# Optimization experiments

Hardware: AMD Instinct MI355X
Metric: run time of the kernel (lower is better)

## Reference

```python
import jax, jax.numpy as jnp
import numpy as np

N_NODES = 50000
N_EDGES = 400000
NFEAT, NHID, NOUT, NCLASS = 512, 256, 256, 8


def _glorot(key, shape):
    lim = float(np.sqrt(6.0 / (shape[0] + shape[1])))
    return jax.random.uniform(key, shape, jnp.float32, -lim, lim)


def setup_inputs() -> dict:
    key = jax.random.key(0)
    ks = jax.random.split(key, 8)
    x = jax.random.normal(ks[0], (N_NODES, NFEAT), jnp.float32)
    edge_index = jax.random.randint(ks[1], (2, N_EDGES), 0, N_NODES, jnp.int32)
    # learnable edge weight logits (init 1 - eps in the module; trained => generic values)
    edge_w_params = jnp.ones((N_EDGES,), jnp.float32) * 0.9999
    W1 = _glorot(ks[2], (NFEAT, NHID)); b1 = jnp.zeros((NHID,), jnp.float32)
    W2 = _glorot(ks[3], (NHID, NHID)); b2 = jnp.zeros((NHID,), jnp.float32)
    W3 = _glorot(ks[4], (NHID, NOUT)); b3 = jnp.zeros((NOUT,), jnp.float32)
    Wlin = _glorot(ks[5], (NHID + NHID + NOUT, NCLASS))
    blin = jnp.zeros((NCLASS,), jnp.float32)
    return {"x": x, "edge_index": edge_index, "edge_w_params": edge_w_params,
            "W1": W1, "b1": b1, "W2": W2, "b2": b2, "W3": W3, "b3": b3,
            "Wlin": Wlin, "blin": blin}


def _gcn_conv(x, W, b, src, dst, ew, n):
    """PyG GCNConv with add_self_loops=True.
    Self-loop weight is 1 (fill_value). norm = d^-1/2[src] * w * d^-1/2[dst].
    Self-loop contribution handled analytically (no edge concat).
    """
    deg = jax.ops.segment_sum(ew, dst, num_segments=n) + 1.0  # +1 self-loop weight
    dinv = jnp.where(deg > 0, jax.lax.rsqrt(deg), 0.0)
    norm = dinv[src] * ew * dinv[dst]                          # [E]
    h = x @ W                                                  # [n, out]
    agg = jax.ops.segment_sum(h[src] * norm[:, None], dst, num_segments=n)
    agg = agg + h * (dinv * dinv)[:, None]                     # self loops
    return agg + b


def reference(x, edge_index, edge_w_params, W1, b1, W2, b2, W3, b3, Wlin, blin):
    n = x.shape[0]
    src, dst = edge_index[0], edge_index[1]
    ew = jax.nn.sigmoid(edge_w_params)
    ones_ew = jnp.ones_like(ew)
    x1 = jax.nn.relu(_gcn_conv(x, W1, b1, src, dst, ew, n))    # dropout: eval mode (identity)
    x2 = jax.nn.relu(_gcn_conv(x1, W2, b2, src, dst, ew, n))
    x3 = _gcn_conv(x2, W3, b3, src, dst, ones_ew, n)           # gc3 called without edge_weight
    logits = jnp.concatenate((x1, x2, x3), axis=1) @ Wlin + blin
    return jax.nn.log_softmax(logits, axis=1)
```

## Files before the change

kernel.cpp:

```cpp
#include <hip/hip_runtime.h>
#include <math.h>

#define N_NODES 50000
#define N_EDGES 400000
#define M_PAD 50048
#define NFEAT 512
#define NHID 256
#define NCLASS 8
#define SCAN_BLOCKS ((N_NODES + 255) / 256)

typedef unsigned short u16;
typedef __attribute__((ext_vector_type(8))) unsigned short u16x8;
typedef __attribute__((ext_vector_type(8))) short s16x8;
typedef __attribute__((ext_vector_type(4))) float f32x4;

__device__ __forceinline__ float bf2f(u16 u) {
    union { unsigned int i; float f; } v; v.i = ((unsigned int)u) << 16; return v.f;
}
__device__ __forceinline__ float bf2f_hi(unsigned int packed) {
    union { unsigned int i; float f; } v; v.i = packed & 0xffff0000u; return v.f;
}
__device__ __forceinline__ float bf2f_lo(unsigned int packed) {
    union { unsigned int i; float f; } v; v.i = packed << 16; return v.f;
}
__device__ __forceinline__ u16 f2bf(float f) {
    union { float f; unsigned int i; } v; v.f = f;
    unsigned int r = v.i + 0x7fffu + ((v.i >> 16) & 1u);
    return (u16)(r >> 16);
}


__global__ void init_k(float* deg, int* cnt, int* cur) {
    int i = blockIdx.x * blockDim.x + threadIdx.x;
    if (i < N_NODES) { deg[i] = 1.0f; cnt[i] = 0; cur[i] = 0; }
}

__global__ void edge_deg_k(const float* __restrict__ p, const int* __restrict__ dst,
                           float* __restrict__ deg, int* __restrict__ cnt,
                           float* __restrict__ ew_out) {
    int e = blockIdx.x * blockDim.x + threadIdx.x;
    if (e >= N_EDGES) return;
    float ew = 1.0f / (1.0f + expf(-p[e]));
    ew_out[e] = ew;
    int d = dst[e];
    atomicAdd(&deg[d], ew);
    atomicAdd(&cnt[d], 1);
}

__global__ void finalize_dinv_k(float* __restrict__ deg, const int* __restrict__ cnt,
                                float* __restrict__ dinv3) {
    int i = blockIdx.x * blockDim.x + threadIdx.x;
    if (i < N_NODES) {
        deg[i]   = 1.0f / sqrtf(deg[i]);
        dinv3[i] = 1.0f / sqrtf(1.0f + (float)cnt[i]);
    }
}

__global__ __launch_bounds__(256) void scan1_k(const int* __restrict__ cnt,
                                               int* __restrict__ row_start,
                                               int* __restrict__ bsum) {
    __shared__ int tmp[256];
    int t = threadIdx.x;
    int g = blockIdx.x * 256 + t;
    int v = (g < N_NODES) ? cnt[g] : 0;
    tmp[t] = v;
    __syncthreads();
    #pragma unroll
    for (int off = 1; off < 256; off <<= 1) {
        int u = (t >= off) ? tmp[t - off] : 0;
        __syncthreads();
        tmp[t] += u;
        __syncthreads();
    }
    if (g < N_NODES) row_start[g] = tmp[t] - v;
    if (t == 255) bsum[blockIdx.x] = tmp[255];
}

__global__ __launch_bounds__(256) void scan2_k(int* __restrict__ bsum) {
    __shared__ int tmp[256];
    int t = threadIdx.x;
    int v = (t < SCAN_BLOCKS) ? bsum[t] : 0;
    tmp[t] = v;
    __syncthreads();
    #pragma unroll
    for (int off = 1; off < 256; off <<= 1) {
        int u = (t >= off) ? tmp[t - off] : 0;
        __syncthreads();
        tmp[t] += u;
        __syncthreads();
    }
    if (t < SCAN_BLOCKS) bsum[t] = tmp[t] - v;
}

__global__ __launch_bounds__(256) void scan3_k(int* __restrict__ row_start,
                                               const int* __restrict__ bsum) {
    int t = threadIdx.x;
    int g = blockIdx.x * 256 + t;
    if (g < N_NODES) row_start[g] += bsum[blockIdx.x];
    if (g == 0) row_start[N_NODES] = N_EDGES;
}

__global__ void fill_k(const int* __restrict__ src, const int* __restrict__ dst,
                       const float* __restrict__ ew, const float* __restrict__ dinv,
                       const float* __restrict__ dinv3,
                       const int* __restrict__ row_start, int* __restrict__ cur,
                       uint2* __restrict__ ep, uint2* __restrict__ ep3) {
    int e = blockIdx.x * blockDim.x + threadIdx.x;
    if (e >= N_EDGES) return;
    int s = src[e], d = dst[e];
    float w  = dinv[s] * ew[e] * dinv[d];
    float w3 = dinv3[s] * dinv3[d];
    int p = atomicAdd(&cur[d], 1);
    int slot = row_start[d] + p;
    ep[slot]  = make_uint2((unsigned int)s, __float_as_uint(w));
    ep3[slot] = make_uint2((unsigned int)s, __float_as_uint(w3));
}


__global__ void convx_k(const float* __restrict__ x, u16* __restrict__ xb) {
    int idx = blockIdx.x * 256 + threadIdx.x;
    if (idx >= M_PAD * (NFEAT / 8)) return;
    int row = idx >> 6;
    size_t e0 = (size_t)idx * 8;
    u16x8 o = {0, 0, 0, 0, 0, 0, 0, 0};
    if (row < N_NODES) {
        float4 a = *(const float4*)&x[e0];
        float4 b = *(const float4*)&x[e0 + 4];
        o[0] = f2bf(a.x); o[1] = f2bf(a.y); o[2] = f2bf(a.z); o[3] = f2bf(a.w);
        o[4] = f2bf(b.x); o[5] = f2bf(b.y); o[6] = f2bf(b.z); o[7] = f2bf(b.w);
    }
    *(u16x8*)&xb[e0] = o;
}

__global__ void wtrans_k(const float* __restrict__ W, u16* __restrict__ Wt, int K) {
    int idx = blockIdx.x * 256 + threadIdx.x;
    if (idx >= 256 * K) return;
    int n = idx / K, k = idx - n * K;
    Wt[idx] = f2bf(W[(size_t)k * 256 + n]);
}

__global__ void zeropad_k(u16* a, u16* b) {
    int i = blockIdx.x * 256 + threadIdx.x;
    if (i < (M_PAD - N_NODES) * 256) {
        a[(size_t)N_NODES * 256 + i] = 0;
        b[(size_t)N_NODES * 256 + i] = 0;
    }
}


__global__ __launch_bounds__(256) void gemm_bf16_k(const u16* __restrict__ A,
                                                   const u16* __restrict__ BT,
                                                   u16* __restrict__ C, int K) {
    __shared__ u16 Asl[128 * 40];
    __shared__ u16 Bsl[128 * 40];
    int tid = threadIdx.x;
    int lane = tid & 63;
    int wid = tid >> 6;
    int wm = wid >> 1, wn = wid & 1;
    int row0 = blockIdx.x * 128;
    int col0 = blockIdx.y * 128;

    int c0 = tid, c1 = tid + 256;
    int ar0 = c0 >> 2, ak0 = (c0 & 3) << 3;
    int ar1 = c1 >> 2, ak1 = (c1 & 3) << 3;
    const u16* Ag0 = A + (size_t)(row0 + ar0) * K + ak0;
    const u16* Ag1 = A + (size_t)(row0 + ar1) * K + ak1;
    const u16* Bg0 = BT + (size_t)(col0 + ar0) * K + ak0;
    const u16* Bg1 = BT + (size_t)(col0 + ar1) * K + ak1;
    int la0 = ar0 * 40 + ak0, la1 = ar1 * 40 + ak1;

    u16x8 ra0 = *(const u16x8*)Ag0;
    u16x8 ra1 = *(const u16x8*)Ag1;
    u16x8 rb0 = *(const u16x8*)Bg0;
    u16x8 rb1 = *(const u16x8*)Bg1;

    f32x4 acc[4][4] = {};

    int arow = wm * 64 + (lane & 15);
    int bcol = wn * 64 + (lane & 15);
    int kg = (lane >> 4) << 3;

    int nt = K >> 5;
    for (int t = 0; t < nt; ++t) {
        __syncthreads();
        *(u16x8*)&Asl[la0] = ra0; *(u16x8*)&Asl[la1] = ra1;
        *(u16x8*)&Bsl[la0] = rb0; *(u16x8*)&Bsl[la1] = rb1;
        __syncthreads();
        if (t + 1 < nt) {
            int ko = (t + 1) << 5;
            ra0 = *(const u16x8*)(Ag0 + ko);
            ra1 = *(const u16x8*)(Ag1 + ko);
            rb0 = *(const u16x8*)(Bg0 + ko);
            rb1 = *(const u16x8*)(Bg1 + ko);
        }
        s16x8 af[4], bf[4];
        #pragma unroll
        for (int m = 0; m < 4; ++m)
            af[m] = *(const s16x8*)&Asl[(arow + m * 16) * 40 + kg];
        #pragma unroll
        for (int n = 0; n < 4; ++n)
            bf[n] = *(const s16x8*)&Bsl[(bcol + n * 16) * 40 + kg];
        #pragma unroll
        for (int m = 0; m < 4; ++m)
            #pragma unroll
            for (int n = 0; n < 4; ++n)
                acc[m][n] = __builtin_amdgcn_mfma_f32_16x16x32_bf16(af[m], bf[n], acc[m][n], 0, 0, 0);
    }

    int crow0 = row0 + wm * 64 + ((lane >> 4) << 2);
    int ccol  = col0 + wn * 64 + (lane & 15);
    #pragma unroll
    for (int m = 0; m < 4; ++m)
        #pragma unroll
        for (int n = 0; n < 4; ++n)
            #pragma unroll
            for (int r = 0; r < 4; ++r)
                C[(size_t)(crow0 + m * 16 + r) * 256 + ccol + n * 16] = f2bf(acc[m][n][r]);
}


template <bool RELU>
__global__ __launch_bounds__(256) void gather_k(const u16* __restrict__ h,
                                                const int* __restrict__ row_start,
                                                const uint2* __restrict__ ep,
                                                const float* __restrict__ dinv,
                                                const float* __restrict__ bias,
                                                u16* __restrict__ outb) {
    int node = blockIdx.x * 4 + (threadIdx.x >> 6);
    if (node >= N_NODES) return;
    int lane = threadIdx.x & 63;

    float di = dinv[node];
    float sw = di * di;
    uint2 hv = *(const uint2*)(h + (size_t)node * 256 + lane * 4);
    float4 acc;
    acc.x = bf2f_lo(hv.x) * sw; acc.y = bf2f_hi(hv.x) * sw;
    acc.z = bf2f_lo(hv.y) * sw; acc.w = bf2f_hi(hv.y) * sw;

    int beg = row_start[node], end = row_start[node + 1];
    for (int j = beg; j < end; ++j) {
        uint2 e = ep[j];
        float w = __uint_as_float(e.y);
        uint2 uv = *(const uint2*)(h + (size_t)e.x * 256 + lane * 4);
        acc.x += bf2f_lo(uv.x) * w; acc.y += bf2f_hi(uv.x) * w;
        acc.z += bf2f_lo(uv.y) * w; acc.w += bf2f_hi(uv.y) * w;
    }
    float4 bv = ((const float4*)bias)[lane];
    acc.x += bv.x; acc.y += bv.y; acc.z += bv.z; acc.w += bv.w;
    if (RELU) {
        acc.x = fmaxf(acc.x, 0.f); acc.y = fmaxf(acc.y, 0.f);
        acc.z = fmaxf(acc.z, 0.f); acc.w = fmaxf(acc.w, 0.f);
    }
    uint2 o;
    o.x = (unsigned int)f2bf(acc.x) | ((unsigned int)f2bf(acc.y) << 16);
    o.y = (unsigned int)f2bf(acc.z) | ((unsigned int)f2bf(acc.w) << 16);
    *(uint2*)(outb + (size_t)node * 256 + lane * 4) = o;
}


template <bool FIRST>
__global__ __launch_bounds__(256) void logits_acc_k(const u16* __restrict__ x,
                                                    const float* __restrict__ Wlin,
                                                    const float* __restrict__ blin,
                                                    float* __restrict__ logits, int seg) {
    __shared__ float Ws[256 * 8];
    int tid = threadIdx.x;
    const float* Wseg = Wlin + (size_t)seg * 256 * 8;
    for (int i = tid; i < 2048; i += 256) Ws[i] = Wseg[i];
    __syncthreads();
    int row = blockIdx.x * 32 + (tid >> 3);
    int c = tid & 7;
    if (row >= N_NODES) return;
    const u16* xr = x + (size_t)row * 256;
    float acc = 0.f;
    for (int k8 = 0; k8 < 32; ++k8) {
        u16x8 v = *(const u16x8*)&xr[k8 * 8];
        #pragma unroll
        for (int i = 0; i < 8; ++i) acc += bf2f(v[i]) * Ws[(k8 * 8 + i) * 8 + c];
    }
    float* lp = &logits[(size_t)row * 8 + c];
    if (FIRST) *lp = acc + blin[c];
    else       *lp += acc;
}

__global__ void log_softmax_k(const float* __restrict__ logits, float* __restrict__ out) {
    int row = blockIdx.x * blockDim.x + threadIdx.x;
    if (row >= N_NODES) return;
    float4 a = *(const float4*)&logits[(size_t)row * 8];
    float4 b = *(const float4*)&logits[(size_t)row * 8 + 4];
    float m = fmaxf(fmaxf(fmaxf(a.x, a.y), fmaxf(a.z, a.w)),
                    fmaxf(fmaxf(b.x, b.y), fmaxf(b.z, b.w)));
    float s = expf(a.x - m) + expf(a.y - m) + expf(a.z - m) + expf(a.w - m)
            + expf(b.x - m) + expf(b.y - m) + expf(b.z - m) + expf(b.w - m);
    float ls = logf(s) + m;
    float* o = &out[(size_t)row * 8];
    o[0] = a.x - ls; o[1] = a.y - ls; o[2] = a.z - ls; o[3] = a.w - ls;
    o[4] = b.x - ls; o[5] = b.y - ls; o[6] = b.z - ls; o[7] = b.w - ls;
}


extern "C" void kernel_launch(void* const* d_in, const int* in_sizes, int n_in,
                              void* d_out, int out_size, void* d_ws, size_t ws_size,
                              hipStream_t stream) {
    const float* x    = (const float*)d_in[0];
    const int*   ei   = (const int*)d_in[1];
    const float* ewp  = (const float*)d_in[2];
    const float* W1   = (const float*)d_in[3];
    const float* b1   = (const float*)d_in[4];
    const float* W2   = (const float*)d_in[5];
    const float* b2   = (const float*)d_in[6];
    const float* W3   = (const float*)d_in[7];
    const float* b3   = (const float*)d_in[8];
    const float* Wlin = (const float*)d_in[9];
    const float* blin = (const float*)d_in[10];
    float* out = (float*)d_out;

    const int* src = ei;
    const int* dst = ei + N_EDGES;

    float* ws = (float*)d_ws;
    float* ew     = ws;
    float* dinv   = ew + N_EDGES;
    float* dinv3  = dinv + N_NODES;
    float* logits = dinv3 + N_NODES;
    int* cnt       = (int*)(logits + (size_t)N_NODES * 8);
    int* cur       = cnt + N_NODES;
    int* row_start = cur + N_NODES;
    int* bsum      = row_start + N_NODES + 1;
    uint2* ep  = (uint2*)(((uintptr_t)(bsum + SCAN_BLOCKS) + 127) & ~(uintptr_t)127);
    uint2* ep3 = ep + N_EDGES;
    u16* xb  = (u16*)(ep3 + N_EDGES);
    u16* hb  = xb  + (size_t)M_PAD * 512;
    u16* x1b = hb  + (size_t)M_PAD * 256;
    u16* x2b = x1b + (size_t)M_PAD * 256;
    u16* x3b = x2b + (size_t)M_PAD * 256;
    u16* wt1 = x3b + (size_t)M_PAD * 256;
    u16* wt2 = wt1 + 256 * 512;
    u16* wt3 = wt2 + 256 * 256;

    dim3 blk(256);
    int nodeBlocks  = (N_NODES + 255) / 256;
    int edgeBlocks  = (N_EDGES + 255) / 256;
    int gathBlocks  = (N_NODES + 3) / 4;
    int rowBlocks32 = (N_NODES + 31) / 32;
    dim3 gemmGrid(M_PAD / 128, 2);

    init_k<<<nodeBlocks, blk, 0, stream>>>(dinv, cnt, cur);
    edge_deg_k<<<edgeBlocks, blk, 0, stream>>>(ewp, dst, dinv, cnt, ew);
    finalize_dinv_k<<<nodeBlocks, blk, 0, stream>>>(dinv, cnt, dinv3);
    scan1_k<<<SCAN_BLOCKS, blk, 0, stream>>>(cnt, row_start, bsum);
    scan2_k<<<1, blk, 0, stream>>>(bsum);
    scan3_k<<<SCAN_BLOCKS, blk, 0, stream>>>(row_start, bsum);
    fill_k<<<edgeBlocks, blk, 0, stream>>>(src, dst, ew, dinv, dinv3, row_start, cur, ep, ep3);

    convx_k<<<M_PAD * (NFEAT / 8) / 256, blk, 0, stream>>>(x, xb);
    wtrans_k<<<NFEAT, blk, 0, stream>>>(W1, wt1, NFEAT);
    wtrans_k<<<NHID, blk, 0, stream>>>(W2, wt2, NHID);
    wtrans_k<<<NHID, blk, 0, stream>>>(W3, wt3, NHID);
    zeropad_k<<<48, blk, 0, stream>>>(x1b, x2b);

    gemm_bf16_k<<<gemmGrid, blk, 0, stream>>>(xb, wt1, hb, NFEAT);
    gather_k<true><<<gathBlocks, blk, 0, stream>>>(hb, row_start, ep, dinv, b1, x1b);
    logits_acc_k<true><<<rowBlocks32, blk, 0, stream>>>(x1b, Wlin, blin, logits, 0);

    gemm_bf16_k<<<gemmGrid, blk, 0, stream>>>(x1b, wt2, hb, NHID);
    gather_k<true><<<gathBlocks, blk, 0, stream>>>(hb, row_start, ep, dinv, b2, x2b);
    logits_acc_k<false><<<rowBlocks32, blk, 0, stream>>>(x2b, Wlin, blin, logits, 1);

    gemm_bf16_k<<<gemmGrid, blk, 0, stream>>>(x2b, wt3, hb, NHID);
    gather_k<false><<<gathBlocks, blk, 0, stream>>>(hb, row_start, ep3, dinv3, b3, x3b);
    logits_acc_k<false><<<rowBlocks32, blk, 0, stream>>>(x3b, Wlin, blin, logits, 2);

    log_softmax_k<<<nodeBlocks, blk, 0, stream>>>(logits, out);
}
```

Baseline: 374.1 us.

## Fuse x conversion into GEMM and logits/log-softmax into gather kernels

```diff
diff --git a/kernel.cpp b/kernel.cpp
--- a/kernel.cpp
+++ b/kernel.cpp
@@ -14,9 +14,6 @@
 typedef __attribute__((ext_vector_type(8))) short s16x8;
 typedef __attribute__((ext_vector_type(4))) float f32x4;
 
-__device__ __forceinline__ float bf2f(u16 u) {
-    union { unsigned int i; float f; } v; v.i = ((unsigned int)u) << 16; return v.f;
-}
 __device__ __forceinline__ float bf2f_hi(unsigned int packed) {
     union { unsigned int i; float f; } v; v.i = packed & 0xffff0000u; return v.f;
 }
@@ -117,26 +114,17 @@
 }
 
 
-__global__ void convx_k(const float* __restrict__ x, u16* __restrict__ xb) {
+__global__ void wtrans_all_k(const float* __restrict__ W1, const float* __restrict__ W2,
+                             const float* __restrict__ W3, u16* __restrict__ wt1,
+                             u16* __restrict__ wt2, u16* __restrict__ wt3) {
     int idx = blockIdx.x * 256 + threadIdx.x;
-    if (idx >= M_PAD * (NFEAT / 8)) return;
-    int row = idx >> 6;
-    size_t e0 = (size_t)idx * 8;
-    u16x8 o = {0, 0, 0, 0, 0, 0, 0, 0};
-    if (row < N_NODES) {
-        float4 a = *(const float4*)&x[e0];
-        float4 b = *(const float4*)&x[e0 + 4];
-        o[0] = f2bf(a.x); o[1] = f2bf(a.y); o[2] = f2bf(a.z); o[3] = f2bf(a.w);
-        o[4] = f2bf(b.x); o[5] = f2bf(b.y); o[6] = f2bf(b.z); o[7] = f2bf(b.w);
-    }
-    *(u16x8*)&xb[e0] = o;
-}
-
-__global__ void wtrans_k(const float* __restrict__ W, u16* __restrict__ Wt, int K) {
-    int idx = blockIdx.x * 256 + threadIdx.x;
-    if (idx >= 256 * K) return;
+    const float* W; u16* Wt; int K;
+    if (idx < 256 * 512)           { W = W1; Wt = wt1; K = 512; }
+    else if (idx < 256 * 512 + 256 * 256) { idx -= 256 * 512; W = W2; Wt = wt2; K = 256; }
+    else if (idx < 256 * 512 + 2 * 256 * 256) { idx -= 256 * 512 + 256 * 256; W = W3; Wt = wt3; K = 256; }
+    else return;
     int n = idx / K, k = idx - n * K;
-    Wt[idx] = f2bf(W[(size_t)k * 256 + n]);
+    Wt[(size_t)n * K + k] = f2bf(W[(size_t)k * 256 + n]);
 }
 
 __global__ void zeropad_k(u16* a, u16* b) {
@@ -148,7 +136,19 @@
 }
 
 
-__global__ __launch_bounds__(256) void gemm_bf16_k(const u16* __restrict__ A,
+__device__ __forceinline__ u16x8 ldcvt_f32(const float* p, bool ok) {
+    u16x8 o = {0, 0, 0, 0, 0, 0, 0, 0};
+    if (ok) {
+        float4 a = *(const float4*)p;
+        float4 b = *(const float4*)(p + 4);
+        o[0] = f2bf(a.x); o[1] = f2bf(a.y); o[2] = f2bf(a.z); o[3] = f2bf(a.w);
+        o[4] = f2bf(b.x); o[5] = f2bf(b.y); o[6] = f2bf(b.z); o[7] = f2bf(b.w);
+    }
+    return o;
+}
+
+template <bool AF32>
+__global__ __launch_bounds__(256) void gemm_bf16_k(const void* __restrict__ Ap,
                                                    const u16* __restrict__ BT,
                                                    u16* __restrict__ C, int K) {
     __shared__ u16 Asl[128 * 40];
@@ -163,14 +163,21 @@
     int c0 = tid, c1 = tid + 256;
     int ar0 = c0 >> 2, ak0 = (c0 & 3) << 3;
     int ar1 = c1 >> 2, ak1 = (c1 & 3) << 3;
-    const u16* Ag0 = A + (size_t)(row0 + ar0) * K + ak0;
-    const u16* Ag1 = A + (size_t)(row0 + ar1) * K + ak1;
+    const u16*   A16 = (const u16*)Ap;
+    const float* A32 = (const float*)Ap;
+    bool ok0 = (row0 + ar0) < N_NODES;
+    bool ok1 = (row0 + ar1) < N_NODES;
+    const u16* Ag0 = A16 + (size_t)(row0 + ar0) * K + ak0;
+    const u16* Ag1 = A16 + (size_t)(row0 + ar1) * K + ak1;
+    const float* Af0 = A32 + (size_t)(row0 + ar0) * K + ak0;
+    const float* Af1 = A32 + (size_t)(row0 + ar1) * K + ak1;
     const u16* Bg0 = BT + (size_t)(col0 + ar0) * K + ak0;
     const u16* Bg1 = BT + (size_t)(col0 + ar1) * K + ak1;
     int la0 = ar0 * 40 + ak0, la1 = ar1 * 40 + ak1;
 
-    u16x8 ra0 = *(const u16x8*)Ag0;
-    u16x8 ra1 = *(const u16x8*)Ag1;
+    u16x8 ra0, ra1;
+    if (AF32) { ra0 = ldcvt_f32(Af0, ok0); ra1 = ldcvt_f32(Af1, ok1); }
+    else      { ra0 = *(const u16x8*)Ag0;  ra1 = *(const u16x8*)Ag1; }
     u16x8 rb0 = *(const u16x8*)Bg0;
     u16x8 rb1 = *(const u16x8*)Bg1;
 
@@ -188,8 +195,8 @@
         __syncthreads();
         if (t + 1 < nt) {
             int ko = (t + 1) << 5;
-            ra0 = *(const u16x8*)(Ag0 + ko);
-            ra1 = *(const u16x8*)(Ag1 + ko);
+            if (AF32) { ra0 = ldcvt_f32(Af0 + ko, ok0); ra1 = ldcvt_f32(Af1 + ko, ok1); }
+            else      { ra0 = *(const u16x8*)(Ag0 + ko); ra1 = *(const u16x8*)(Ag1 + ko); }
             rb0 = *(const u16x8*)(Bg0 + ko);
             rb1 = *(const u16x8*)(Bg1 + ko);
         }
@@ -219,16 +226,30 @@
 }
 
 
-template <bool RELU>
+template <int MODE>
 __global__ __launch_bounds__(256) void gather_k(const u16* __restrict__ h,
                                                 const int* __restrict__ row_start,
                                                 const uint2* __restrict__ ep,
                                                 const float* __restrict__ dinv,
                                                 const float* __restrict__ bias,
-                                                u16* __restrict__ outb) {
+                                                const float* __restrict__ Wlin,
+                                                const float* __restrict__ blin,
+                                                u16* __restrict__ outb,
+                                                float* __restrict__ logits,
+                                                float* __restrict__ out) {
     int node = blockIdx.x * 4 + (threadIdx.x >> 6);
     if (node >= N_NODES) return;
     int lane = threadIdx.x & 63;
+
+    const float* Wseg = Wlin + MODE * 2048 + 32 * lane;
+    float4 wv0 = *(const float4*)&Wseg[0];
+    float4 wv1 = *(const float4*)&Wseg[4];
+    float4 wv2 = *(const float4*)&Wseg[8];
+    float4 wv3 = *(const float4*)&Wseg[12];
+    float4 wv4 = *(const float4*)&Wseg[16];
+    float4 wv5 = *(const float4*)&Wseg[20];
+    float4 wv6 = *(const float4*)&Wseg[24];
+    float4 wv7 = *(const float4*)&Wseg[28];
 
     float di = dinv[node];
     float sw = di * di;
@@ -247,55 +268,59 @@
     }
     float4 bv = ((const float4*)bias)[lane];
     acc.x += bv.x; acc.y += bv.y; acc.z += bv.z; acc.w += bv.w;
-    if (RELU) {
+    if (MODE != 2) {
         acc.x = fmaxf(acc.x, 0.f); acc.y = fmaxf(acc.y, 0.f);
         acc.z = fmaxf(acc.z, 0.f); acc.w = fmaxf(acc.w, 0.f);
-    }
-    uint2 o;
-    o.x = (unsigned int)f2bf(acc.x) | ((unsigned int)f2bf(acc.y) << 16);
-    o.y = (unsigned int)f2bf(acc.z) | ((unsigned int)f2bf(acc.w) << 16);
-    *(uint2*)(outb + (size_t)node * 256 + lane * 4) = o;
-}
-
-
-template <bool FIRST>
-__global__ __launch_bounds__(256) void logits_acc_k(const u16* __restrict__ x,
-                                                    const float* __restrict__ Wlin,
-                                                    const float* __restrict__ blin,
-                                                    float* __restrict__ logits, int seg) {
-    __shared__ float Ws[256 * 8];
-    int tid = threadIdx.x;
-    const float* Wseg = Wlin + (size_t)seg * 256 * 8;
-    for (int i = tid; i < 2048; i += 256) Ws[i] = Wseg[i];
-    __syncthreads();
-    int row = blockIdx.x * 32 + (tid >> 3);
-    int c = tid & 7;
-    if (row >= N_NODES) return;
-    const u16* xr = x + (size_t)row * 256;
-    float acc = 0.f;
-    for (int k8 = 0; k8 < 32; ++k8) {
-        u16x8 v = *(const u16x8*)&xr[k8 * 8];
-        #pragma unroll
-        for (int i = 0; i < 8; ++i) acc += bf2f(v[i]) * Ws[(k8 * 8 + i) * 8 + c];
-    }
-    float* lp = &logits[(size_t)row * 8 + c];
-    if (FIRST) *lp = acc + blin[c];
-    else       *lp += acc;
-}
-
-__global__ void log_softmax_k(const float* __restrict__ logits, float* __restrict__ out) {
-    int row = blockIdx.x * blockDim.x + threadIdx.x;
-    if (row >= N_NODES) return;
-    float4 a = *(const float4*)&logits[(size_t)row * 8];
-    float4 b = *(const float4*)&logits[(size_t)row * 8 + 4];
-    float m = fmaxf(fmaxf(fmaxf(a.x, a.y), fmaxf(a.z, a.w)),
-                    fmaxf(fmaxf(b.x, b.y), fmaxf(b.z, b.w)));
-    float s = expf(a.x - m) + expf(a.y - m) + expf(a.z - m) + expf(a.w - m)
-            + expf(b.x - m) + expf(b.y - m) + expf(b.z - m) + expf(b.w - m);
-    float ls = logf(s) + m;
-    float* o = &out[(size_t)row * 8];
-    o[0] = a.x - ls; o[1] = a.y - ls; o[2] = a.z - ls; o[3] = a.w - ls;
-    o[4] = b.x - ls; o[5] = b.y - ls; o[6] = b.z - ls; o[7] = b.w - ls;
+        uint2 o;
+        o.x = (unsigned int)f2bf(acc.x) | ((unsigned int)f2bf(acc.y) << 16);
+        o.y = (unsigned int)f2bf(acc.z) | ((unsigned int)f2bf(acc.w) << 16);
+        *(uint2*)(outb + (size_t)node * 256 + lane * 4) = o;
+    }
+
+    float p0 = acc.x * wv0.x + acc.y * wv2.x + acc.z * wv4.x + acc.w * wv6.x;
+    float p1 = acc.x * wv0.y + acc.y * wv2.y + acc.z * wv4.y + acc.w * wv6.y;
+    float p2 = acc.x * wv0.z + acc.y * wv2.z + acc.z * wv4.z + acc.w * wv6.z;
+    float p3 = acc.x * wv0.w + acc.y * wv2.w + acc.z * wv4.w + acc.w * wv6.w;
+    float p4 = acc.x * wv1.x + acc.y * wv3.x + acc.z * wv5.x + acc.w * wv7.x;
+    float p5 = acc.x * wv1.y + acc.y * wv3.y + acc.z * wv5.y + acc.w * wv7.y;
+    float p6 = acc.x * wv1.z + acc.y * wv3.z + acc.z * wv5.z + acc.w * wv7.z;
+    float p7 = acc.x * wv1.w + acc.y * wv3.w + acc.z * wv5.w + acc.w * wv7.w;
+
+    #pragma unroll
+    for (int off = 1; off < 64; off <<= 1) {
+        p0 += __shfl_xor(p0, off); p1 += __shfl_xor(p1, off);
+        p2 += __shfl_xor(p2, off); p3 += __shfl_xor(p3, off);
+        p4 += __shfl_xor(p4, off); p5 += __shfl_xor(p5, off);
+        p6 += __shfl_xor(p6, off); p7 += __shfl_xor(p7, off);
+    }
+
+    if (lane == 0) {
+        float* lp = &logits[(size_t)node * 8];
+        if (MODE == 0) {
+            float4 bl0 = *(const float4*)&blin[0];
+            float4 bl1 = *(const float4*)&blin[4];
+            *(float4*)&lp[0] = make_float4(p0 + bl0.x, p1 + bl0.y, p2 + bl0.z, p3 + bl0.w);
+            *(float4*)&lp[4] = make_float4(p4 + bl1.x, p5 + bl1.y, p6 + bl1.z, p7 + bl1.w);
+        } else if (MODE == 1) {
+            float4 l0 = *(const float4*)&lp[0];
+            float4 l1 = *(const float4*)&lp[4];
+            *(float4*)&lp[0] = make_float4(l0.x + p0, l0.y + p1, l0.z + p2, l0.w + p3);
+            *(float4*)&lp[4] = make_float4(l1.x + p4, l1.y + p5, l1.z + p6, l1.w + p7);
+        } else {
+            float4 l0 = *(const float4*)&lp[0];
+            float4 l1 = *(const float4*)&lp[4];
+            float t0 = l0.x + p0, t1 = l0.y + p1, t2 = l0.z + p2, t3 = l0.w + p3;
+            float t4 = l1.x + p4, t5 = l1.y + p5, t6 = l1.z + p6, t7 = l1.w + p7;
+            float m = fmaxf(fmaxf(fmaxf(t0, t1), fmaxf(t2, t3)),
+                            fmaxf(fmaxf(t4, t5), fmaxf(t6, t7)));
+            float s = expf(t0 - m) + expf(t1 - m) + expf(t2 - m) + expf(t3 - m)
+                    + expf(t4 - m) + expf(t5 - m) + expf(t6 - m) + expf(t7 - m);
+            float ls = logf(s) + m;
+            float* o = &out[(size_t)node * 8];
+            *(float4*)&o[0] = make_float4(t0 - ls, t1 - ls, t2 - ls, t3 - ls);
+            *(float4*)&o[4] = make_float4(t4 - ls, t5 - ls, t6 - ls, t7 - ls);
+        }
+    }
 }
 
 
@@ -329,20 +354,17 @@
     int* bsum      = row_start + N_NODES + 1;
     uint2* ep  = (uint2*)(((uintptr_t)(bsum + SCAN_BLOCKS) + 127) & ~(uintptr_t)127);
     uint2* ep3 = ep + N_EDGES;
-    u16* xb  = (u16*)(ep3 + N_EDGES);
-    u16* hb  = xb  + (size_t)M_PAD * 512;
+    u16* hb  = (u16*)(ep3 + N_EDGES);
     u16* x1b = hb  + (size_t)M_PAD * 256;
     u16* x2b = x1b + (size_t)M_PAD * 256;
-    u16* x3b = x2b + (size_t)M_PAD * 256;
-    u16* wt1 = x3b + (size_t)M_PAD * 256;
+    u16* wt1 = x2b + (size_t)M_PAD * 256;
     u16* wt2 = wt1 + 256 * 512;
     u16* wt3 = wt2 + 256 * 256;
 
     dim3 blk(256);
-    int nodeBlocks  = (N_NODES + 255) / 256;
-    int edgeBlocks  = (N_EDGES + 255) / 256;
-    int gathBlocks  = (N_NODES + 3) / 4;
-    int rowBlocks32 = (N_NODES + 31) / 32;
+    int nodeBlocks = (N_NODES + 255) / 256;
+    int edgeBlocks = (N_EDGES + 255) / 256;
+    int gathBlocks = (N_NODES + 3) / 4;
     dim3 gemmGrid(M_PAD / 128, 2);
 
     init_k<<<nodeBlocks, blk, 0, stream>>>(dinv, cnt, cur);
@@ -353,23 +375,19 @@
     scan3_k<<<SCAN_BLOCKS, blk, 0, stream>>>(row_start, bsum);
     fill_k<<<edgeBlocks, blk, 0, stream>>>(src, dst, ew, dinv, dinv3, row_start, cur, ep, ep3);
 
-    convx_k<<<M_PAD * (NFEAT / 8) / 256, blk, 0, stream>>>(x, xb);
-    wtrans_k<<<NFEAT, blk, 0, stream>>>(W1, wt1, NFEAT);
-    wtrans_k<<<NHID, blk, 0, stream>>>(W2, wt2, NHID);
-    wtrans_k<<<NHID, blk, 0, stream>>>(W3, wt3, NHID);
+    wtrans_all_k<<<(256 * 512 + 2 * 256 * 256 + 255) / 256, blk, 0, stream>>>(
+        W1, W2, W3, wt1, wt2, wt3);
     zeropad_k<<<48, blk, 0, stream>>>(x1b, x2b);
 
-    gemm_bf16_k<<<gemmGrid, blk, 0, stream>>>(xb, wt1, hb, NFEAT);
-    gather_k<true><<<gathBlocks, blk, 0, stream>>>(hb, row_start, ep, dinv, b1, x1b);
-    logits_acc_k<true><<<rowBlocks32, blk, 0, stream>>>(x1b, Wlin, blin, logits, 0);
-
-    gemm_bf16_k<<<gemmGrid, blk, 0, stream>>>(x1b, wt2, hb, NHID);
-    gather_k<true><<<gathBlocks, blk, 0, stream>>>(hb, row_start, ep, dinv, b2, x2b);
-    logits_acc_k<false><<<rowBlocks32, blk, 0, stream>>>(x2b, Wlin, blin, logits, 1);
-
-    gemm_bf16_k<<<gemmGrid, blk, 0, stream>>>(x2b, wt3, hb, NHID);
-    gather_k<false><<<gathBlocks, blk, 0, stream>>>(hb, row_start, ep3, dinv3, b3, x3b);
-    logits_acc_k<false><<<rowBlocks32, blk, 0, stream>>>(x3b, Wlin, blin, logits, 2);
-
-    log_softmax_k<<<nodeBlocks, blk, 0, stream>>>(logits, out);
-}
+    gemm_bf16_k<true><<<gemmGrid, blk, 0, stream>>>(x, wt1, hb, NFEAT);
+    gather_k<0><<<gathBlocks, blk, 0, stream>>>(hb, row_start, ep, dinv, b1,
+                                                Wlin, blin, x1b, logits, nullptr);
+
+    gemm_bf16_k<false><<<gemmGrid, blk, 0, stream>>>(x1b, wt2, hb, NHID);
+    gather_k<1><<<gathBlocks, blk, 0, stream>>>(hb, row_start, ep, dinv, b2,
+                                                Wlin, blin, x2b, logits, nullptr);
+
+    gemm_bf16_k<false><<<gemmGrid, blk, 0, stream>>>(x2b, wt3, hb, NHID);
+    gather_k<2><<<gathBlocks, blk, 0, stream>>>(hb, row_start, ep3, dinv3, b3,
+                                                Wlin, blin, nullptr, logits, out);
+}
```

Result: slower. 454.3 us (+21.4%).

## Fuse fp32-to-bf16 input conversion into first GEMM, merge weight transposes, unroll gather

Applied to the files above, without the earlier changes.

```diff
diff --git a/kernel.cpp b/kernel.cpp
--- a/kernel.cpp
+++ b/kernel.cpp
@@ -117,26 +117,17 @@
 }
 
 
-__global__ void convx_k(const float* __restrict__ x, u16* __restrict__ xb) {
+__global__ void wtrans_all_k(const float* __restrict__ W1, const float* __restrict__ W2,
+                             const float* __restrict__ W3, u16* __restrict__ wt1,
+                             u16* __restrict__ wt2, u16* __restrict__ wt3) {
     int idx = blockIdx.x * 256 + threadIdx.x;
-    if (idx >= M_PAD * (NFEAT / 8)) return;
-    int row = idx >> 6;
-    size_t e0 = (size_t)idx * 8;
-    u16x8 o = {0, 0, 0, 0, 0, 0, 0, 0};
-    if (row < N_NODES) {
-        float4 a = *(const float4*)&x[e0];
-        float4 b = *(const float4*)&x[e0 + 4];
-        o[0] = f2bf(a.x); o[1] = f2bf(a.y); o[2] = f2bf(a.z); o[3] = f2bf(a.w);
-        o[4] = f2bf(b.x); o[5] = f2bf(b.y); o[6] = f2bf(b.z); o[7] = f2bf(b.w);
-    }
-    *(u16x8*)&xb[e0] = o;
-}
-
-__global__ void wtrans_k(const float* __restrict__ W, u16* __restrict__ Wt, int K) {
-    int idx = blockIdx.x * 256 + threadIdx.x;
-    if (idx >= 256 * K) return;
+    const float* W; u16* Wt; int K;
+    if (idx < 256 * 512)           { W = W1; Wt = wt1; K = 512; }
+    else if (idx < 256 * 512 + 256 * 256) { idx -= 256 * 512; W = W2; Wt = wt2; K = 256; }
+    else if (idx < 256 * 512 + 2 * 256 * 256) { idx -= 256 * 512 + 256 * 256; W = W3; Wt = wt3; K = 256; }
+    else return;
     int n = idx / K, k = idx - n * K;
-    Wt[idx] = f2bf(W[(size_t)k * 256 + n]);
+    Wt[(size_t)n * K + k] = f2bf(W[(size_t)k * 256 + n]);
 }
 
 __global__ void zeropad_k(u16* a, u16* b) {
@@ -148,7 +139,19 @@
 }
 
 
-__global__ __launch_bounds__(256) void gemm_bf16_k(const u16* __restrict__ A,
+__device__ __forceinline__ u16x8 ldcvt_f32(const float* p, bool ok) {
+    u16x8 o = {0, 0, 0, 0, 0, 0, 0, 0};
+    if (ok) {
+        float4 a = *(const float4*)p;
+        float4 b = *(const float4*)(p + 4);
+        o[0] = f2bf(a.x); o[1] = f2bf(a.y); o[2] = f2bf(a.z); o[3] = f2bf(a.w);
+        o[4] = f2bf(b.x); o[5] = f2bf(b.y); o[6] = f2bf(b.z); o[7] = f2bf(b.w);
+    }
+    return o;
+}
+
+template <bool AF32>
+__global__ __launch_bounds__(256) void gemm_bf16_k(const void* __restrict__ Ap,
                                                    const u16* __restrict__ BT,
                                                    u16* __restrict__ C, int K) {
     __shared__ u16 Asl[128 * 40];
@@ -163,14 +166,21 @@
     int c0 = tid, c1 = tid + 256;
     int ar0 = c0 >> 2, ak0 = (c0 & 3) << 3;
     int ar1 = c1 >> 2, ak1 = (c1 & 3) << 3;
-    const u16* Ag0 = A + (size_t)(row0 + ar0) * K + ak0;
-    const u16* Ag1 = A + (size_t)(row0 + ar1) * K + ak1;
+    const u16*   A16 = (const u16*)Ap;
+    const float* A32 = (const float*)Ap;
+    bool ok0 = (row0 + ar0) < N_NODES;
+    bool ok1 = (row0 + ar1) < N_NODES;
+    const u16* Ag0 = A16 + (size_t)(row0 + ar0) * K + ak0;
+    const u16* Ag1 = A16 + (size_t)(row0 + ar1) * K + ak1;
+    const float* Af0 = A32 + (size_t)(row0 + ar0) * K + ak0;
+    const float* Af1 = A32 + (size_t)(row0 + ar1) * K + ak1;
     const u16* Bg0 = BT + (size_t)(col0 + ar0) * K + ak0;
     const u16* Bg1 = BT + (size_t)(col0 + ar1) * K + ak1;
     int la0 = ar0 * 40 + ak0, la1 = ar1 * 40 + ak1;
 
-    u16x8 ra0 = *(const u16x8*)Ag0;
-    u16x8 ra1 = *(const u16x8*)Ag1;
+    u16x8 ra0, ra1;
+    if (AF32) { ra0 = ldcvt_f32(Af0, ok0); ra1 = ldcvt_f32(Af1, ok1); }
+    else      { ra0 = *(const u16x8*)Ag0;  ra1 = *(const u16x8*)Ag1; }
     u16x8 rb0 = *(const u16x8*)Bg0;
     u16x8 rb1 = *(const u16x8*)Bg1;
 
@@ -188,8 +198,8 @@
         __syncthreads();
         if (t + 1 < nt) {
             int ko = (t + 1) << 5;
-            ra0 = *(const u16x8*)(Ag0 + ko);
-            ra1 = *(const u16x8*)(Ag1 + ko);
+            if (AF32) { ra0 = ldcvt_f32(Af0 + ko, ok0); ra1 = ldcvt_f32(Af1 + ko, ok1); }
+            else      { ra0 = *(const u16x8*)(Ag0 + ko); ra1 = *(const u16x8*)(Ag1 + ko); }
             rb0 = *(const u16x8*)(Bg0 + ko);
             rb1 = *(const u16x8*)(Bg1 + ko);
         }
@@ -238,7 +248,25 @@
     acc.z = bf2f_lo(hv.y) * sw; acc.w = bf2f_hi(hv.y) * sw;
 
     int beg = row_start[node], end = row_start[node + 1];
-    for (int j = beg; j < end; ++j) {
+    int j = beg;
+    for (; j + 4 <= end; j += 4) {
+        uint2 e0 = ep[j], e1 = ep[j + 1], e2 = ep[j + 2], e3 = ep[j + 3];
+        uint2 u0 = *(const uint2*)(h + (size_t)e0.x * 256 + lane * 4);
+        uint2 u1 = *(const uint2*)(h + (size_t)e1.x * 256 + lane * 4);
+        uint2 u2 = *(const uint2*)(h + (size_t)e2.x * 256 + lane * 4);
+        uint2 u3 = *(const uint2*)(h + (size_t)e3.x * 256 + lane * 4);
+        float w0 = __uint_as_float(e0.y), w1 = __uint_as_float(e1.y);
+        float w2 = __uint_as_float(e2.y), w3 = __uint_as_float(e3.y);
+        acc.x += bf2f_lo(u0.x) * w0; acc.y += bf2f_hi(u0.x) * w0;
+        acc.z += bf2f_lo(u0.y) * w0; acc.w += bf2f_hi(u0.y) * w0;
+        acc.x += bf2f_lo(u1.x) * w1; acc.y += bf2f_hi(u1.x) * w1;
+        acc.z += bf2f_lo(u1.y) * w1; acc.w += bf2f_hi(u1.y) * w1;
+        acc.x += bf2f_lo(u2.x) * w2; acc.y += bf2f_hi(u2.x) * w2;
+        acc.z += bf2f_lo(u2.y) * w2; acc.w += bf2f_hi(u2.y) * w2;
+        acc.x += bf2f_lo(u3.x) * w3; acc.y += bf2f_hi(u3.x) * w3;
+        acc.z += bf2f_lo(u3.y) * w3; acc.w += bf2f_hi(u3.y) * w3;
+    }
+    for (; j < end; ++j) {
         uint2 e = ep[j];
         float w = __uint_as_float(e.y);
         uint2 uv = *(const uint2*)(h + (size_t)e.x * 256 + lane * 4);
@@ -329,8 +357,7 @@
     int* bsum      = row_start + N_NODES + 1;
     uint2* ep  = (uint2*)(((uintptr_t)(bsum + SCAN_BLOCKS) + 127) & ~(uintptr_t)127);
     uint2* ep3 = ep + N_EDGES;
-    u16* xb  = (u16*)(ep3 + N_EDGES);
-    u16* hb  = xb  + (size_t)M_PAD * 512;
+    u16* hb  = (u16*)(ep3 + N_EDGES);
     u16* x1b = hb  + (size_t)M_PAD * 256;
     u16* x2b = x1b + (size_t)M_PAD * 256;
     u16* x3b = x2b + (size_t)M_PAD * 256;
@@ -353,21 +380,19 @@
     scan3_k<<<SCAN_BLOCKS, blk, 0, stream>>>(row_start, bsum);
     fill_k<<<edgeBlocks, blk, 0, stream>>>(src, dst, ew, dinv, dinv3, row_start, cur, ep, ep3);
 
-    convx_k<<<M_PAD * (NFEAT / 8) / 256, blk, 0, stream>>>(x, xb);
-    wtrans_k<<<NFEAT, blk, 0, stream>>>(W1, wt1, NFEAT);
-    wtrans_k<<<NHID, blk, 0, stream>>>(W2, wt2, NHID);
-    wtrans_k<<<NHID, blk, 0, stream>>>(W3, wt3, NHID);
+    wtrans_all_k<<<(256 * 512 + 2 * 256 * 256 + 255) / 256, blk, 0, stream>>>(
+        W1, W2, W3, wt1, wt2, wt3);
     zeropad_k<<<48, blk, 0, stream>>>(x1b, x2b);
 
-    gemm_bf16_k<<<gemmGrid, blk, 0, stream>>>(xb, wt1, hb, NFEAT);
+    gemm_bf16_k<true><<<gemmGrid, blk, 0, stream>>>(x, wt1, hb, NFEAT);
     gather_k<true><<<gathBlocks, blk, 0, stream>>>(hb, row_start, ep, dinv, b1, x1b);
     logits_acc_k<true><<<rowBlocks32, blk, 0, stream>>>(x1b, Wlin, blin, logits, 0);
 
-    gemm_bf16_k<<<gemmGrid, blk, 0, stream>>>(x1b, wt2, hb, NHID);
+    gemm_bf16_k<false><<<gemmGrid, blk, 0, stream>>>(x1b, wt2, hb, NHID);
     gather_k<true><<<gathBlocks, blk, 0, stream>>>(hb, row_start, ep, dinv, b2, x2b);
     logits_acc_k<false><<<rowBlocks32, blk, 0, stream>>>(x2b, Wlin, blin, logits, 1);
 
-    gemm_bf16_k<<<gemmGrid, blk, 0, stream>>>(x2b, wt3, hb, NHID);
+    gemm_bf16_k<false><<<gemmGrid, blk, 0, stream>>>(x2b, wt3, hb, NHID);
     gather_k<false><<<gathBlocks, blk, 0, stream>>>(hb, row_start, ep3, dinv3, b3, x3b);
     logits_acc_k<false><<<rowBlocks32, blk, 0, stream>>>(x3b, Wlin, blin, logits, 2);
 
```

Result: faster. 319.1 us (-14.7%).
